# Optimization experiments

Measured on AMD Instinct MI355X. Metric: run time of the kernel, lower is better.

## Reference

```python
import jax, jax.numpy as jnp
import numpy as np

N, E = 50000, 800000
IN_D, HID, H1, OUT_D, H2, EDGE_D = 64, 16, 8, 64, 2, 1
NEG_SLOPE = 0.2


def gatv2_layer(x, src, dst, edge_attr, Wl, Wr, We, att, bias, concat):
    """PyG GATv2Conv (add_self_loops=False, share_weights=False), eval mode (no dropout)."""
    n = x.shape[0]
    H, C = att.shape
    xl = (x @ Wl).reshape(n, H, C)            # source transform
    xr = (x @ Wr).reshape(n, H, C)            # target transform
    ee = (edge_attr @ We).reshape(-1, H, C)   # edge embedding
    z = jax.nn.leaky_relu(xl[src] + xr[dst] + ee, NEG_SLOPE)  # [E,H,C]
    score = jnp.einsum('ehc,hc->eh', z, att)                  # [E,H]
    # softmax over incoming edges per target node
    m = jax.ops.segment_max(score, dst, num_segments=n)
    m = jnp.where(jnp.isfinite(m), m, 0.0)
    a = jnp.exp(score - m[dst])
    denom = jax.ops.segment_sum(a, dst, num_segments=n)
    alpha = a / (denom[dst] + 1e-16)                          # [E,H]
    msg = xl[src] * alpha[..., None]                          # [E,H,C]
    out = jax.ops.segment_sum(msg, dst, num_segments=n)       # [N,H,C]
    if concat:
        return out.reshape(n, H * C) + bias
    return out.mean(axis=1) + bias


def layer_norm(x, g, b):
    mu = x.mean(-1, keepdims=True)
    var = ((x - mu) ** 2).mean(-1, keepdims=True)
    return (x - mu) * jax.lax.rsqrt(var + 1e-5) * g + b


def setup_inputs() -> dict:
    key = jax.random.key(0)
    ks = jax.random.split(key, 24)
    def w(k, *shape):
        fan_in = shape[0]
        return jax.random.normal(k, shape, dtype=jnp.float32) * (1.0 / np.sqrt(fan_in))
    inp = {
        'x': jax.random.normal(ks[0], (N, IN_D), dtype=jnp.float32),
        'edge_index': jax.random.randint(ks[1], (2, E), 0, N, dtype=jnp.int64),
        'edge_attr': jax.random.normal(ks[2], (E, EDGE_D), dtype=jnp.float32),
        # layer 1 (heads=8, out=16, concat)
        'w1_l': w(ks[3], IN_D, H1 * HID), 'w1_r': w(ks[4], IN_D, H1 * HID),
        'w1_e': w(ks[5], EDGE_D, H1 * HID),
        'att1': jax.random.normal(ks[6], (H1, HID), dtype=jnp.float32) * 0.1,
        'b1': jnp.zeros((H1 * HID,), dtype=jnp.float32),
        # layer 2 (heads=2, out=64, mean)
        'w2_l': w(ks[7], H1 * HID, H2 * OUT_D), 'w2_r': w(ks[8], H1 * HID, H2 * OUT_D),
        'w2_e': w(ks[9], EDGE_D, H2 * OUT_D),
        'att2': jax.random.normal(ks[10], (H2, OUT_D), dtype=jnp.float32) * 0.1,
        'b2': jnp.zeros((OUT_D,), dtype=jnp.float32),
        # classifier: Linear + LayerNorm + GELU + ResidualBlockv2
        'wc': w(ks[11], OUT_D, OUT_D), 'bc': jnp.zeros((OUT_D,), dtype=jnp.float32),
        'ln_g': jnp.ones((OUT_D,), dtype=jnp.float32), 'ln_b': jnp.zeros((OUT_D,), dtype=jnp.float32),
        'wr': w(ks[12], OUT_D, OUT_D), 'br': jnp.zeros((OUT_D,), dtype=jnp.float32),
        'lnr_g': jnp.ones((OUT_D,), dtype=jnp.float32), 'lnr_b': jnp.zeros((OUT_D,), dtype=jnp.float32),
    }
    return inp


def reference(x, edge_index, edge_attr, w1_l, w1_r, w1_e, att1, b1,
              w2_l, w2_r, w2_e, att2, b2, wc, bc, ln_g, ln_b, wr, br, lnr_g, lnr_b):
    src, dst = edge_index[0], edge_index[1]
    h = jax.nn.relu(gatv2_layer(x, src, dst, edge_attr, w1_l, w1_r, w1_e, att1, b1, True))
    h = jax.nn.relu(gatv2_layer(h, src, dst, edge_attr, w2_l, w2_r, w2_e, att2, b2, False))
    h = jax.nn.gelu(layer_norm(h @ wc + bc, ln_g, ln_b), approximate=False)
    # ResidualBlockv2: Linear -> LayerNorm -> GELU with residual skip
    h = h + jax.nn.gelu(layer_norm(h @ wr + br, lnr_g, lnr_b), approximate=False)
    return h
```

## Files before the change

kernel.cpp:

```cpp
#include <hip/hip_runtime.h>
#include <math.h>

#define NNODE 50000
#define NEDGE 800000
#define NBLK_SCAN 196

__device__ __forceinline__ float wsum64(float v) {
    #pragma unroll
    for (int m = 32; m >= 1; m >>= 1) v += __shfl_xor(v, m, 64);
    return v;
}

__device__ __forceinline__ float gelu_exact(float x) {
    return 0.5f * x * (1.0f + erff(x * 0.70710678118654752f));
}

__device__ __forceinline__ float lrelu(float z) { return z > 0.f ? z : 0.2f * z; }

__global__ void fill_u32(unsigned* __restrict__ p, unsigned v, int n) {
    int i = blockIdx.x * blockDim.x + threadIdx.x;
    if (i < n) p[i] = v;
}

__global__ __launch_bounds__(256) void build_deg(const int* __restrict__ ei, int* __restrict__ deg) {
    int e = blockIdx.x * 256 + threadIdx.x;
    if (e >= NEDGE) return;
    atomicAdd(&deg[ei[NEDGE + e]], 1);
}

__global__ __launch_bounds__(256) void scan1(const int* __restrict__ deg,
                                             int* __restrict__ partial,
                                             int* __restrict__ bsum) {
    __shared__ int tmp[256];
    int t = threadIdx.x;
    int gid = blockIdx.x * 256 + t;
    int v = (gid < NNODE) ? deg[gid] : 0;
    tmp[t] = v;
    __syncthreads();
    #pragma unroll
    for (int off = 1; off < 256; off <<= 1) {
        int u = (t >= off) ? tmp[t - off] : 0;
        __syncthreads();
        tmp[t] += u;
        __syncthreads();
    }
    if (gid < NNODE) partial[gid] = tmp[t] - v;
    if (t == 255) bsum[blockIdx.x] = tmp[255];
}

__global__ __launch_bounds__(256) void scan2(int* __restrict__ bsum, int* __restrict__ boff) {
    __shared__ int tmp[256];
    int t = threadIdx.x;
    int v = (t < NBLK_SCAN) ? bsum[t] : 0;
    tmp[t] = v;
    __syncthreads();
    #pragma unroll
    for (int off = 1; off < 256; off <<= 1) {
        int u = (t >= off) ? tmp[t - off] : 0;
        __syncthreads();
        tmp[t] += u;
        __syncthreads();
    }
    if (t < NBLK_SCAN) boff[t] = tmp[t] - v;
}

__global__ __launch_bounds__(256) void scan3(const int* __restrict__ partial,
                                             const int* __restrict__ boff,
                                             int* __restrict__ base,
                                             int* __restrict__ cursor) {
    int gid = blockIdx.x * 256 + threadIdx.x;
    if (gid < NNODE) {
        int b = partial[gid] + boff[blockIdx.x];
        base[gid] = b;
        cursor[gid] = b;
    }
    if (gid == 0) base[NNODE] = NEDGE;
}

__global__ __launch_bounds__(256) void scatter_edges(const int* __restrict__ ei,
                                                     const float* __restrict__ ea,
                                                     int* __restrict__ cursor,
                                                     int2* __restrict__ se) {
    int e = blockIdx.x * 256 + threadIdx.x;
    if (e >= NEDGE) return;
    int d = ei[NEDGE + e];
    int i = atomicAdd(&cursor[d], 1);
    se[i] = make_int2(ei[e], __float_as_int(ea[e]));
}

template<int K>
__global__ __launch_bounds__(256) void node_xform(const float* __restrict__ in,
                                                  const float* __restrict__ wl,
                                                  const float* __restrict__ wr,
                                                  float* __restrict__ xl,
                                                  float* __restrict__ xr) {
    __shared__ float xrow[32][K];
    int t = threadIdx.x;
    int n0 = blockIdx.x * 32;
    for (int idx = t; idx < 32 * (K / 4); idx += 256) {
        int row = idx / (K / 4), c4 = idx % (K / 4);
        float4 v = make_float4(0.f, 0.f, 0.f, 0.f);
        if (n0 + row < NNODE) v = ((const float4*)(in + (size_t)(n0 + row) * K))[c4];
        ((float4*)xrow[row])[c4] = v;
    }
    __syncthreads();
    int cg = t & 63, ns = t >> 6;
    const float* wsel = (cg < 32) ? wl : wr;
    float* osel = (cg < 32) ? xl : xr;
    int ccol = (cg & 31) * 4;
    const float* wp = wsel + ccol;
    const float* xbase = xrow[ns * 8];
    float4 acc[8];
    #pragma unroll
    for (int k = 0; k < 8; ++k) acc[k] = make_float4(0.f, 0.f, 0.f, 0.f);
    for (int i = 0; i < K; i += 4) {
        float4 w0 = *(const float4*)(wp + (size_t)(i + 0) * 128);
        float4 w1 = *(const float4*)(wp + (size_t)(i + 1) * 128);
        float4 w2 = *(const float4*)(wp + (size_t)(i + 2) * 128);
        float4 w3 = *(const float4*)(wp + (size_t)(i + 3) * 128);
        #pragma unroll
        for (int k = 0; k < 8; ++k) {
            float4 xv = *(const float4*)(xbase + (size_t)k * K + i);
            acc[k].x += xv.x * w0.x + xv.y * w1.x + xv.z * w2.x + xv.w * w3.x;
            acc[k].y += xv.x * w0.y + xv.y * w1.y + xv.z * w2.y + xv.w * w3.y;
            acc[k].z += xv.x * w0.z + xv.y * w1.z + xv.z * w2.z + xv.w * w3.z;
            acc[k].w += xv.x * w0.w + xv.y * w1.w + xv.z * w2.w + xv.w * w3.w;
        }
    }
    #pragma unroll
    for (int k = 0; k < 8; ++k) {
        int n = n0 + ns * 8 + k;
        if (n < NNODE) *(float4*)(osel + (size_t)n * 128 + ccol) = acc[k];
    }
}

__global__ __launch_bounds__(256) void fused1(const int* __restrict__ base,
                                              const int2* __restrict__ se,
                                              const float* __restrict__ xl,
                                              const float* __restrict__ xr,
                                              const float* __restrict__ w1e,
                                              const float* __restrict__ att1,
                                              const float* __restrict__ b1,
                                              float* __restrict__ h1) {
    int t = threadIdx.x;
    int wv = t >> 6, ln = t & 63;
    int half = ln >> 5, sub = ln & 31;
    int n = blockIdx.x * 4 + wv;
    int ch = sub * 4;
    float4 xrv = *(const float4*)(xr + (size_t)n * 128 + ch);
    float4 wev = *(const float4*)(w1e + ch);
    float4 atv = *(const float4*)(att1 + ch);
    int i0 = base[n], i1 = base[n + 1];
    float m = -1e30f, den = 0.f;
    float4 o = make_float4(0.f, 0.f, 0.f, 0.f);
    int i = i0 + half;
    if (i < i1) {
        int2 r = se[i];
        float4 xv = *(const float4*)(xl + (size_t)r.x * 128 + ch);
        float a = __int_as_float(r.y);
        for (i += 2; i < i1; i += 2) {
            int2 rn = se[i];
            float4 nxv = *(const float4*)(xl + (size_t)rn.x * 128 + ch);
            float na = __int_as_float(rn.y);
            float part = lrelu(fmaf(a, wev.x, xv.x + xrv.x)) * atv.x
                       + lrelu(fmaf(a, wev.y, xv.y + xrv.y)) * atv.y
                       + lrelu(fmaf(a, wev.z, xv.z + xrv.z)) * atv.z
                       + lrelu(fmaf(a, wev.w, xv.w + xrv.w)) * atv.w;
            part += __shfl_xor(part, 1, 64);
            part += __shfl_xor(part, 2, 64);
            float mn = fmaxf(m, part);
            float sc = __expf(m - mn);
            float p  = __expf(part - mn);
            den = den * sc + p;
            o.x = o.x * sc + p * xv.x;
            o.y = o.y * sc + p * xv.y;
            o.z = o.z * sc + p * xv.z;
            o.w = o.w * sc + p * xv.w;
            m = mn;
            xv = nxv; a = na;
        }
        float part = lrelu(fmaf(a, wev.x, xv.x + xrv.x)) * atv.x
                   + lrelu(fmaf(a, wev.y, xv.y + xrv.y)) * atv.y
                   + lrelu(fmaf(a, wev.z, xv.z + xrv.z)) * atv.z
                   + lrelu(fmaf(a, wev.w, xv.w + xrv.w)) * atv.w;
        part += __shfl_xor(part, 1, 64);
        part += __shfl_xor(part, 2, 64);
        float mn = fmaxf(m, part);
        float sc = __expf(m - mn);
        float p  = __expf(part - mn);
        den = den * sc + p;
        o.x = o.x * sc + p * xv.x;
        o.y = o.y * sc + p * xv.y;
        o.z = o.z * sc + p * xv.z;
        o.w = o.w * sc + p * xv.w;
        m = mn;
    }
    float m2   = __shfl_xor(m, 32, 64);
    float den2 = __shfl_xor(den, 32, 64);
    float4 o2;
    o2.x = __shfl_xor(o.x, 32, 64);
    o2.y = __shfl_xor(o.y, 32, 64);
    o2.z = __shfl_xor(o.z, 32, 64);
    o2.w = __shfl_xor(o.w, 32, 64);
    float mn = fmaxf(m, m2);
    float s1 = __expf(m - mn), s2 = __expf(m2 - mn);
    den = den * s1 + den2 * s2;
    float inv = 1.f / (den + 1e-16f);
    if (half == 0) {
        float4 bv = *(const float4*)(b1 + ch);
        float4 res;
        res.x = fmaxf((o.x * s1 + o2.x * s2) * inv + bv.x, 0.f);
        res.y = fmaxf((o.y * s1 + o2.y * s2) * inv + bv.y, 0.f);
        res.z = fmaxf((o.z * s1 + o2.z * s2) * inv + bv.z, 0.f);
        res.w = fmaxf((o.w * s1 + o2.w * s2) * inv + bv.w, 0.f);
        *(float4*)(h1 + (size_t)n * 128 + ch) = res;
    }
}

__global__ __launch_bounds__(256) void fused2(const int* __restrict__ base,
                                              const int2* __restrict__ se,
                                              const float* __restrict__ xl,
                                              const float* __restrict__ xr,
                                              const float* __restrict__ w2e,
                                              const float* __restrict__ att2,
                                              const float* __restrict__ b2,
                                              float* __restrict__ h2) {
    int t = threadIdx.x;
    int wv = t >> 6, ln = t & 63;
    int half = ln >> 5, sub = ln & 31;
    int n = blockIdx.x * 4 + wv;
    int ch = sub * 4;
    float4 xrv = *(const float4*)(xr + (size_t)n * 128 + ch);
    float4 wev = *(const float4*)(w2e + ch);
    float4 atv = *(const float4*)(att2 + ch);
    int i0 = base[n], i1 = base[n + 1];
    float m = -1e30f, den = 0.f;
    float4 o = make_float4(0.f, 0.f, 0.f, 0.f);
    int i = i0 + half;
    if (i < i1) {
        int2 r = se[i];
        float4 xv = *(const float4*)(xl + (size_t)r.x * 128 + ch);
        float a = __int_as_float(r.y);
        for (i += 2; i < i1; i += 2) {
            int2 rn = se[i];
            float4 nxv = *(const float4*)(xl + (size_t)rn.x * 128 + ch);
            float na = __int_as_float(rn.y);
            float part = lrelu(fmaf(a, wev.x, xv.x + xrv.x)) * atv.x
                       + lrelu(fmaf(a, wev.y, xv.y + xrv.y)) * atv.y
                       + lrelu(fmaf(a, wev.z, xv.z + xrv.z)) * atv.z
                       + lrelu(fmaf(a, wev.w, xv.w + xrv.w)) * atv.w;
            part += __shfl_xor(part, 1, 64);
            part += __shfl_xor(part, 2, 64);
            part += __shfl_xor(part, 4, 64);
            part += __shfl_xor(part, 8, 64);
            float mn = fmaxf(m, part);
            float sc = __expf(m - mn);
            float p  = __expf(part - mn);
            den = den * sc + p;
            o.x = o.x * sc + p * xv.x;
            o.y = o.y * sc + p * xv.y;
            o.z = o.z * sc + p * xv.z;
            o.w = o.w * sc + p * xv.w;
            m = mn;
            xv = nxv; a = na;
        }
        float part = lrelu(fmaf(a, wev.x, xv.x + xrv.x)) * atv.x
                   + lrelu(fmaf(a, wev.y, xv.y + xrv.y)) * atv.y
                   + lrelu(fmaf(a, wev.z, xv.z + xrv.z)) * atv.z
                   + lrelu(fmaf(a, wev.w, xv.w + xrv.w)) * atv.w;
        part += __shfl_xor(part, 1, 64);
        part += __shfl_xor(part, 2, 64);
        part += __shfl_xor(part, 4, 64);
        part += __shfl_xor(part, 8, 64);
        float mn = fmaxf(m, part);
        float sc = __expf(m - mn);
        float p  = __expf(part - mn);
        den = den * sc + p;
        o.x = o.x * sc + p * xv.x;
        o.y = o.y * sc + p * xv.y;
        o.z = o.z * sc + p * xv.z;
        o.w = o.w * sc + p * xv.w;
        m = mn;
    }
    float m2   = __shfl_xor(m, 32, 64);
    float den2 = __shfl_xor(den, 32, 64);
    float4 o2;
    o2.x = __shfl_xor(o.x, 32, 64);
    o2.y = __shfl_xor(o.y, 32, 64);
    o2.z = __shfl_xor(o.z, 32, 64);
    o2.w = __shfl_xor(o.w, 32, 64);
    float mn = fmaxf(m, m2);
    float s1 = __expf(m - mn), s2 = __expf(m2 - mn);
    den = den * s1 + den2 * s2;
    float inv = 1.f / (den + 1e-16f);
    float4 v;
    v.x = (o.x * s1 + o2.x * s2) * inv;
    v.y = (o.y * s1 + o2.y * s2) * inv;
    v.z = (o.z * s1 + o2.z * s2) * inv;
    v.w = (o.w * s1 + o2.w * s2) * inv;
    float4 u;
    u.x = __shfl_xor(v.x, 16, 64);
    u.y = __shfl_xor(v.y, 16, 64);
    u.z = __shfl_xor(v.z, 16, 64);
    u.w = __shfl_xor(v.w, 16, 64);
    if (half == 0 && sub < 16) {
        float4 bv = *(const float4*)(b2 + ch);
        float4 res;
        res.x = fmaxf(0.5f * (v.x + u.x) + bv.x, 0.f);
        res.y = fmaxf(0.5f * (v.y + u.y) + bv.y, 0.f);
        res.z = fmaxf(0.5f * (v.z + u.z) + bv.z, 0.f);
        res.w = fmaxf(0.5f * (v.w + u.w) + bv.w, 0.f);
        *(float4*)(h2 + (size_t)n * 64 + ch) = res;
    }
}

__global__ __launch_bounds__(256) void classifier(const float* __restrict__ h2,
                                                  const float* __restrict__ wc,
                                                  const float* __restrict__ bc,
                                                  const float* __restrict__ lng,
                                                  const float* __restrict__ lnb,
                                                  const float* __restrict__ wr,
                                                  const float* __restrict__ br,
                                                  const float* __restrict__ lrg,
                                                  const float* __restrict__ lrb,
                                                  float* __restrict__ out) {
    __shared__ float rowA[4][64];
    __shared__ float rowB[4][64];
    int t = threadIdx.x;
    int wv = t >> 6, ln = t & 63;
    int n = blockIdx.x * 4 + wv;
    rowA[wv][ln] = h2[(size_t)n * 64 + ln];
    __syncthreads();
    float acc = bc[ln];
    #pragma unroll 8
    for (int i = 0; i < 64; ++i) acc += rowA[wv][i] * wc[i * 64 + ln];
    float mu = wsum64(acc) * (1.f / 64.f);
    float dv = acc - mu;
    float var = wsum64(dv * dv) * (1.f / 64.f);
    float y = dv * rsqrtf(var + 1e-5f) * lng[ln] + lnb[ln];
    float g1 = gelu_exact(y);
    rowB[wv][ln] = g1;
    __syncthreads();
    float acc2 = br[ln];
    #pragma unroll 8
    for (int i = 0; i < 64; ++i) acc2 += rowB[wv][i] * wr[i * 64 + ln];
    float mu2 = wsum64(acc2) * (1.f / 64.f);
    float dv2 = acc2 - mu2;
    float var2 = wsum64(dv2 * dv2) * (1.f / 64.f);
    float y2 = dv2 * rsqrtf(var2 + 1e-5f) * lrg[ln] + lrb[ln];
    float g2 = gelu_exact(y2);
    out[(size_t)n * 64 + ln] = g1 + g2;
}

extern "C" void kernel_launch(void* const* d_in, const int* in_sizes, int n_in,
                              void* d_out, int out_size, void* d_ws, size_t ws_size,
                              hipStream_t stream) {
    const float* x    = (const float*)d_in[0];
    const int*   ei   = (const int*)d_in[1];
    const float* ea   = (const float*)d_in[2];
    const float* w1l  = (const float*)d_in[3];
    const float* w1r  = (const float*)d_in[4];
    const float* w1e  = (const float*)d_in[5];
    const float* att1 = (const float*)d_in[6];
    const float* b1   = (const float*)d_in[7];
    const float* w2l  = (const float*)d_in[8];
    const float* w2r  = (const float*)d_in[9];
    const float* w2e  = (const float*)d_in[10];
    const float* att2 = (const float*)d_in[11];
    const float* b2   = (const float*)d_in[12];
    const float* wc   = (const float*)d_in[13];
    const float* bc   = (const float*)d_in[14];
    const float* lng  = (const float*)d_in[15];
    const float* lnb  = (const float*)d_in[16];
    const float* wr   = (const float*)d_in[17];
    const float* br   = (const float*)d_in[18];
    const float* lrg  = (const float*)d_in[19];
    const float* lrb  = (const float*)d_in[20];

    float* ws = (float*)d_ws;
    const size_t N128 = (size_t)NNODE * 128;
    float* xl = ws;
    float* xr = xl + N128;
    float* h1 = xr + N128;
    float* h2 = h1 + N128;
    int2*  se      = (int2*)(h2 + (size_t)NNODE * 64);
    int*   deg     = (int*)(se + NEDGE);
    int*   partial = deg + NNODE;
    int*   base    = partial + NNODE;
    int*   cursor  = base + NNODE + 1;
    int*   bsum    = cursor + NNODE;
    int*   boff    = bsum + 256;

    const int EB  = NEDGE / 256;
    const int NBX = (NNODE + 31) / 32;
    const int NB4 = NNODE / 4;

    fill_u32<<<NBLK_SCAN, 256, 0, stream>>>((unsigned*)deg, 0u, NNODE);
    build_deg<<<EB, 256, 0, stream>>>(ei, deg);
    scan1<<<NBLK_SCAN, 256, 0, stream>>>(deg, partial, bsum);
    scan2<<<1, 256, 0, stream>>>(bsum, boff);
    scan3<<<NBLK_SCAN, 256, 0, stream>>>(partial, boff, base, cursor);
    scatter_edges<<<EB, 256, 0, stream>>>(ei, ea, cursor, se);

    node_xform<64><<<NBX, 256, 0, stream>>>(x, w1l, w1r, xl, xr);
    fused1<<<NB4, 256, 0, stream>>>(base, se, xl, xr, w1e, att1, b1, h1);

    node_xform<128><<<NBX, 256, 0, stream>>>(h1, w2l, w2r, xl, xr);
    fused2<<<NB4, 256, 0, stream>>>(base, se, xl, xr, w2e, att2, b2, h2);

    classifier<<<NB4, 256, 0, stream>>>(h2, wc, bc, lng, lnb, wr, br, lrg, lrb,
                                        (float*)d_out);
}
```

Before: 351.6 us.

## Fuse layer-2 aggregation with classifier, widen edge parallelism, single-block scan

The layer-2 GATv2 aggregation kernel and the classifier are merged, so h2 stays in shared memory and its global write and reload go away. Both aggregation kernels now process four edges in parallel per wave with 8 channels per lane, and the online softmax skips the rescale when no lane's score exceeds the running max by more than a threshold. The three-kernel degree scan is replaced by a single-block serial-chunk scan. Risks are the single-block scan being slow, since each thread walks about 196 degrees serially, and higher register pressure from the wider per-lane state.

```diff
diff --git a/kernel.cpp b/kernel.cpp
--- a/kernel.cpp
+++ b/kernel.cpp
@@ -3,7 +3,7 @@
 
 #define NNODE 50000
 #define NEDGE 800000
-#define NBLK_SCAN 196
+#define NBLK 196
 
 __device__ __forceinline__ float wsum64(float v) {
     #pragma unroll
@@ -15,7 +15,63 @@
     return 0.5f * x * (1.0f + erff(x * 0.70710678118654752f));
 }
 
-__device__ __forceinline__ float lrelu(float z) { return z > 0.f ? z : 0.2f * z; }
+__device__ __forceinline__ float part8(float4 xa, float4 xb, float a,
+                                       float4 we0, float4 we1,
+                                       float4 at0, float4 at1,
+                                       float4 xr0, float4 xr1) {
+    float z0 = fmaf(a, we0.x, xa.x + xr0.x);
+    float z1 = fmaf(a, we0.y, xa.y + xr0.y);
+    float z2 = fmaf(a, we0.z, xa.z + xr0.z);
+    float z3 = fmaf(a, we0.w, xa.w + xr0.w);
+    float z4 = fmaf(a, we1.x, xb.x + xr1.x);
+    float z5 = fmaf(a, we1.y, xb.y + xr1.y);
+    float z6 = fmaf(a, we1.z, xb.z + xr1.z);
+    float z7 = fmaf(a, we1.w, xb.w + xr1.w);
+    float s01 = fmaxf(z0, 0.2f * z0) * at0.x + fmaxf(z1, 0.2f * z1) * at0.y;
+    float s23 = fmaxf(z2, 0.2f * z2) * at0.z + fmaxf(z3, 0.2f * z3) * at0.w;
+    float s45 = fmaxf(z4, 0.2f * z4) * at1.x + fmaxf(z5, 0.2f * z5) * at1.y;
+    float s67 = fmaxf(z6, 0.2f * z6) * at1.z + fmaxf(z7, 0.2f * z7) * at1.w;
+    return (s01 + s23) + (s45 + s67);
+}
+
+#define ONLINE_UPDATE(part, xa, xb)                                        \
+    if (__any((part) > m + 8.f)) {                                         \
+        float mn = fmaxf(m, (part));                                       \
+        float sc = __expf(m - mn);                                         \
+        float p  = __expf((part) - mn);                                    \
+        den = den * sc + p;                                                \
+        oa.x = oa.x * sc + p * (xa).x; oa.y = oa.y * sc + p * (xa).y;      \
+        oa.z = oa.z * sc + p * (xa).z; oa.w = oa.w * sc + p * (xa).w;      \
+        ob.x = ob.x * sc + p * (xb).x; ob.y = ob.y * sc + p * (xb).y;      \
+        ob.z = ob.z * sc + p * (xb).z; ob.w = ob.w * sc + p * (xb).w;      \
+        m = mn;                                                            \
+    } else {                                                               \
+        float p = __expf((part) - m);                                      \
+        den += p;                                                          \
+        oa.x = fmaf(p, (xa).x, oa.x); oa.y = fmaf(p, (xa).y, oa.y);        \
+        oa.z = fmaf(p, (xa).z, oa.z); oa.w = fmaf(p, (xa).w, oa.w);        \
+        ob.x = fmaf(p, (xb).x, ob.x); ob.y = fmaf(p, (xb).y, ob.y);        \
+        ob.z = fmaf(p, (xb).z, ob.z); ob.w = fmaf(p, (xb).w, ob.w);        \
+    }
+
+#define MERGE_STATE(D)                                                     \
+    {                                                                      \
+        float m2 = __shfl_xor(m, D, 64);                                   \
+        float d2 = __shfl_xor(den, D, 64);                                 \
+        float4 pa, pb;                                                     \
+        pa.x = __shfl_xor(oa.x, D, 64); pa.y = __shfl_xor(oa.y, D, 64);    \
+        pa.z = __shfl_xor(oa.z, D, 64); pa.w = __shfl_xor(oa.w, D, 64);    \
+        pb.x = __shfl_xor(ob.x, D, 64); pb.y = __shfl_xor(ob.y, D, 64);    \
+        pb.z = __shfl_xor(ob.z, D, 64); pb.w = __shfl_xor(ob.w, D, 64);    \
+        float mn = fmaxf(m, m2);                                           \
+        float s1 = __expf(m - mn), s2 = __expf(m2 - mn);                   \
+        den = den * s1 + d2 * s2;                                          \
+        oa.x = oa.x * s1 + pa.x * s2; oa.y = oa.y * s1 + pa.y * s2;        \
+        oa.z = oa.z * s1 + pa.z * s2; oa.w = oa.w * s1 + pa.w * s2;        \
+        ob.x = ob.x * s1 + pb.x * s2; ob.y = ob.y * s1 + pb.y * s2;        \
+        ob.z = ob.z * s1 + pb.z * s2; ob.w = ob.w * s1 + pb.w * s2;        \
+        m = mn;                                                            \
+    }
 
 __global__ void fill_u32(unsigned* __restrict__ p, unsigned v, int n) {
     int i = blockIdx.x * blockDim.x + threadIdx.x;
@@ -28,53 +84,32 @@
     atomicAdd(&deg[ei[NEDGE + e]], 1);
 }
 
-__global__ __launch_bounds__(256) void scan1(const int* __restrict__ deg,
-                                             int* __restrict__ partial,
-                                             int* __restrict__ bsum) {
-    __shared__ int tmp[256];
+__global__ __launch_bounds__(256) void scan_all(const int* __restrict__ deg,
+                                                int* __restrict__ base,
+                                                int* __restrict__ cursor) {
+    __shared__ int tsum[256];
     int t = threadIdx.x;
-    int gid = blockIdx.x * 256 + t;
-    int v = (gid < NNODE) ? deg[gid] : 0;
-    tmp[t] = v;
+    const int CH = (NNODE + 255) / 256;
+    int s0 = t * CH, s1 = min(s0 + CH, NNODE);
+    int s = 0;
+    for (int i = s0; i < s1; ++i) s += deg[i];
+    tsum[t] = s;
     __syncthreads();
     #pragma unroll
     for (int off = 1; off < 256; off <<= 1) {
-        int u = (t >= off) ? tmp[t - off] : 0;
+        int u = (t >= off) ? tsum[t - off] : 0;
         __syncthreads();
-        tmp[t] += u;
+        tsum[t] += u;
         __syncthreads();
     }
-    if (gid < NNODE) partial[gid] = tmp[t] - v;
-    if (t == 255) bsum[blockIdx.x] = tmp[255];
-}
-
-__global__ __launch_bounds__(256) void scan2(int* __restrict__ bsum, int* __restrict__ boff) {
-    __shared__ int tmp[256];
-    int t = threadIdx.x;
-    int v = (t < NBLK_SCAN) ? bsum[t] : 0;
-    tmp[t] = v;
-    __syncthreads();
-    #pragma unroll
-    for (int off = 1; off < 256; off <<= 1) {
-        int u = (t >= off) ? tmp[t - off] : 0;
-        __syncthreads();
-        tmp[t] += u;
-        __syncthreads();
-    }
-    if (t < NBLK_SCAN) boff[t] = tmp[t] - v;
-}
-
-__global__ __launch_bounds__(256) void scan3(const int* __restrict__ partial,
-                                             const int* __restrict__ boff,
-                                             int* __restrict__ base,
-                                             int* __restrict__ cursor) {
-    int gid = blockIdx.x * 256 + threadIdx.x;
-    if (gid < NNODE) {
-        int b = partial[gid] + boff[blockIdx.x];
-        base[gid] = b;
-        cursor[gid] = b;
-    }
-    if (gid == 0) base[NNODE] = NEDGE;
+    int run = tsum[t] - s;
+    for (int i = s0; i < s1; ++i) {
+        int d = deg[i];
+        base[i] = run;
+        cursor[i] = run;
+        run += d;
+    }
+    if (t == 0) base[NNODE] = NEDGE;
 }
 
 __global__ __launch_bounds__(256) void scatter_edges(const int* __restrict__ ei,
@@ -144,196 +179,147 @@
                                               float* __restrict__ h1) {
     int t = threadIdx.x;
     int wv = t >> 6, ln = t & 63;
-    int half = ln >> 5, sub = ln & 31;
+    int q = ln >> 4, sub = ln & 15;
     int n = blockIdx.x * 4 + wv;
-    int ch = sub * 4;
-    float4 xrv = *(const float4*)(xr + (size_t)n * 128 + ch);
-    float4 wev = *(const float4*)(w1e + ch);
-    float4 atv = *(const float4*)(att1 + ch);
+    int ch = sub * 8;
+    float4 xr0 = *(const float4*)(xr + (size_t)n * 128 + ch);
+    float4 xr1 = *(const float4*)(xr + (size_t)n * 128 + ch + 4);
+    float4 we0 = *(const float4*)(w1e + ch);
+    float4 we1 = *(const float4*)(w1e + ch + 4);
+    float4 at0 = *(const float4*)(att1 + ch);
+    float4 at1 = *(const float4*)(att1 + ch + 4);
     int i0 = base[n], i1 = base[n + 1];
     float m = -1e30f, den = 0.f;
-    float4 o = make_float4(0.f, 0.f, 0.f, 0.f);
-    int i = i0 + half;
+    float4 oa = make_float4(0.f, 0.f, 0.f, 0.f);
+    float4 ob = make_float4(0.f, 0.f, 0.f, 0.f);
+    int i = i0 + q;
     if (i < i1) {
         int2 r = se[i];
-        float4 xv = *(const float4*)(xl + (size_t)r.x * 128 + ch);
+        const float* xp = xl + (size_t)r.x * 128 + ch;
+        float4 xa = *(const float4*)xp, xb = *(const float4*)(xp + 4);
         float a = __int_as_float(r.y);
-        for (i += 2; i < i1; i += 2) {
+        for (i += 4; i < i1; i += 4) {
             int2 rn = se[i];
-            float4 nxv = *(const float4*)(xl + (size_t)rn.x * 128 + ch);
+            const float* xpn = xl + (size_t)rn.x * 128 + ch;
+            float4 nxa = *(const float4*)xpn, nxb = *(const float4*)(xpn + 4);
             float na = __int_as_float(rn.y);
-            float part = lrelu(fmaf(a, wev.x, xv.x + xrv.x)) * atv.x
-                       + lrelu(fmaf(a, wev.y, xv.y + xrv.y)) * atv.y
-                       + lrelu(fmaf(a, wev.z, xv.z + xrv.z)) * atv.z
-                       + lrelu(fmaf(a, wev.w, xv.w + xrv.w)) * atv.w;
+            float part = part8(xa, xb, a, we0, we1, at0, at1, xr0, xr1);
             part += __shfl_xor(part, 1, 64);
-            part += __shfl_xor(part, 2, 64);
-            float mn = fmaxf(m, part);
-            float sc = __expf(m - mn);
-            float p  = __expf(part - mn);
-            den = den * sc + p;
-            o.x = o.x * sc + p * xv.x;
-            o.y = o.y * sc + p * xv.y;
-            o.z = o.z * sc + p * xv.z;
-            o.w = o.w * sc + p * xv.w;
-            m = mn;
-            xv = nxv; a = na;
+            ONLINE_UPDATE(part, xa, xb);
+            xa = nxa; xb = nxb; a = na;
         }
-        float part = lrelu(fmaf(a, wev.x, xv.x + xrv.x)) * atv.x
-                   + lrelu(fmaf(a, wev.y, xv.y + xrv.y)) * atv.y
-                   + lrelu(fmaf(a, wev.z, xv.z + xrv.z)) * atv.z
-                   + lrelu(fmaf(a, wev.w, xv.w + xrv.w)) * atv.w;
+        float part = part8(xa, xb, a, we0, we1, at0, at1, xr0, xr1);
         part += __shfl_xor(part, 1, 64);
-        part += __shfl_xor(part, 2, 64);
-        float mn = fmaxf(m, part);
-        float sc = __expf(m - mn);
-        float p  = __expf(part - mn);
-        den = den * sc + p;
-        o.x = o.x * sc + p * xv.x;
-        o.y = o.y * sc + p * xv.y;
-        o.z = o.z * sc + p * xv.z;
-        o.w = o.w * sc + p * xv.w;
-        m = mn;
-    }
-    float m2   = __shfl_xor(m, 32, 64);
-    float den2 = __shfl_xor(den, 32, 64);
-    float4 o2;
-    o2.x = __shfl_xor(o.x, 32, 64);
-    o2.y = __shfl_xor(o.y, 32, 64);
-    o2.z = __shfl_xor(o.z, 32, 64);
-    o2.w = __shfl_xor(o.w, 32, 64);
-    float mn = fmaxf(m, m2);
-    float s1 = __expf(m - mn), s2 = __expf(m2 - mn);
-    den = den * s1 + den2 * s2;
-    float inv = 1.f / (den + 1e-16f);
-    if (half == 0) {
-        float4 bv = *(const float4*)(b1 + ch);
-        float4 res;
-        res.x = fmaxf((o.x * s1 + o2.x * s2) * inv + bv.x, 0.f);
-        res.y = fmaxf((o.y * s1 + o2.y * s2) * inv + bv.y, 0.f);
-        res.z = fmaxf((o.z * s1 + o2.z * s2) * inv + bv.z, 0.f);
-        res.w = fmaxf((o.w * s1 + o2.w * s2) * inv + bv.w, 0.f);
-        *(float4*)(h1 + (size_t)n * 128 + ch) = res;
-    }
-}
-
-__global__ __launch_bounds__(256) void fused2(const int* __restrict__ base,
-                                              const int2* __restrict__ se,
-                                              const float* __restrict__ xl,
-                                              const float* __restrict__ xr,
-                                              const float* __restrict__ w2e,
-                                              const float* __restrict__ att2,
-                                              const float* __restrict__ b2,
-                                              float* __restrict__ h2) {
+        ONLINE_UPDATE(part, xa, xb);
+    }
+    MERGE_STATE(16);
+    MERGE_STATE(32);
+    if (q == 0) {
+        float inv = 1.f / (den + 1e-16f);
+        float4 bv0 = *(const float4*)(b1 + ch);
+        float4 bv1 = *(const float4*)(b1 + ch + 4);
+        float4 ra, rb;
+        ra.x = fmaxf(oa.x * inv + bv0.x, 0.f);
+        ra.y = fmaxf(oa.y * inv + bv0.y, 0.f);
+        ra.z = fmaxf(oa.z * inv + bv0.z, 0.f);
+        ra.w = fmaxf(oa.w * inv + bv0.w, 0.f);
+        rb.x = fmaxf(ob.x * inv + bv1.x, 0.f);
+        rb.y = fmaxf(ob.y * inv + bv1.y, 0.f);
+        rb.z = fmaxf(ob.z * inv + bv1.z, 0.f);
+        rb.w = fmaxf(ob.w * inv + bv1.w, 0.f);
+        *(float4*)(h1 + (size_t)n * 128 + ch) = ra;
+        *(float4*)(h1 + (size_t)n * 128 + ch + 4) = rb;
+    }
+}
+
+__global__ __launch_bounds__(256) void fused2cls(const int* __restrict__ base,
+                                                 const int2* __restrict__ se,
+                                                 const float* __restrict__ xl,
+                                                 const float* __restrict__ xr,
+                                                 const float* __restrict__ w2e,
+                                                 const float* __restrict__ att2,
+                                                 const float* __restrict__ b2,
+                                                 const float* __restrict__ wc,
+                                                 const float* __restrict__ bc,
+                                                 const float* __restrict__ lng,
+                                                 const float* __restrict__ lnb,
+                                                 const float* __restrict__ wrr,
+                                                 const float* __restrict__ brr,
+                                                 const float* __restrict__ lrg,
+                                                 const float* __restrict__ lrb,
+                                                 float* __restrict__ out) {
+    __shared__ float rowH[4][64];
+    __shared__ float rowB[4][64];
     int t = threadIdx.x;
     int wv = t >> 6, ln = t & 63;
-    int half = ln >> 5, sub = ln & 31;
+    int q = ln >> 4, sub = ln & 15;
     int n = blockIdx.x * 4 + wv;
-    int ch = sub * 4;
-    float4 xrv = *(const float4*)(xr + (size_t)n * 128 + ch);
-    float4 wev = *(const float4*)(w2e + ch);
-    float4 atv = *(const float4*)(att2 + ch);
+    int ch = sub * 8;
+    float4 xr0 = *(const float4*)(xr + (size_t)n * 128 + ch);
+    float4 xr1 = *(const float4*)(xr + (size_t)n * 128 + ch + 4);
+    float4 we0 = *(const float4*)(w2e + ch);
+    float4 we1 = *(const float4*)(w2e + ch + 4);
+    float4 at0 = *(const float4*)(att2 + ch);
+    float4 at1 = *(const float4*)(att2 + ch + 4);
     int i0 = base[n], i1 = base[n + 1];
     float m = -1e30f, den = 0.f;
-    float4 o = make_float4(0.f, 0.f, 0.f, 0.f);
-    int i = i0 + half;
+    float4 oa = make_float4(0.f, 0.f, 0.f, 0.f);
+    float4 ob = make_float4(0.f, 0.f, 0.f, 0.f);
+    int i = i0 + q;
     if (i < i1) {
         int2 r = se[i];
-        float4 xv = *(const float4*)(xl + (size_t)r.x * 128 + ch);
+        const float* xp = xl + (size_t)r.x * 128 + ch;
+        float4 xa = *(const float4*)xp, xb = *(const float4*)(xp + 4);
         float a = __int_as_float(r.y);
-        for (i += 2; i < i1; i += 2) {
+        for (i += 4; i < i1; i += 4) {
             int2 rn = se[i];
-            float4 nxv = *(const float4*)(xl + (size_t)rn.x * 128 + ch);
+            const float* xpn = xl + (size_t)rn.x * 128 + ch;
+            float4 nxa = *(const float4*)xpn, nxb = *(const float4*)(xpn + 4);
             float na = __int_as_float(rn.y);
-            float part = lrelu(fmaf(a, wev.x, xv.x + xrv.x)) * atv.x
-                       + lrelu(fmaf(a, wev.y, xv.y + xrv.y)) * atv.y
-                       + lrelu(fmaf(a, wev.z, xv.z + xrv.z)) * atv.z
-                       + lrelu(fmaf(a, wev.w, xv.w + xrv.w)) * atv.w;
+            float part = part8(xa, xb, a, we0, we1, at0, at1, xr0, xr1);
             part += __shfl_xor(part, 1, 64);
             part += __shfl_xor(part, 2, 64);
             part += __shfl_xor(part, 4, 64);
-            part += __shfl_xor(part, 8, 64);
-            float mn = fmaxf(m, part);
-            float sc = __expf(m - mn);
-            float p  = __expf(part - mn);
-            den = den * sc + p;
-            o.x = o.x * sc + p * xv.x;
-            o.y = o.y * sc + p * xv.y;
-            o.z = o.z * sc + p * xv.z;
-            o.w = o.w * sc + p * xv.w;
-            m = mn;
-            xv = nxv; a = na;
+            ONLINE_UPDATE(part, xa, xb);
+            xa = nxa; xb = nxb; a = na;
         }
-        float part = lrelu(fmaf(a, wev.x, xv.x + xrv.x)) * atv.x
-                   + lrelu(fmaf(a, wev.y, xv.y + xrv.y)) * atv.y
-                   + lrelu(fmaf(a, wev.z, xv.z + xrv.z)) * atv.z
-                   + lrelu(fmaf(a, wev.w, xv.w + xrv.w)) * atv.w;
+        float part = part8(xa, xb, a, we0, we1, at0, at1, xr0, xr1);
         part += __shfl_xor(part, 1, 64);
         part += __shfl_xor(part, 2, 64);
         part += __shfl_xor(part, 4, 64);
-        part += __shfl_xor(part, 8, 64);
-        float mn = fmaxf(m, part);
-        float sc = __expf(m - mn);
-        float p  = __expf(part - mn);
-        den = den * sc + p;
-        o.x = o.x * sc + p * xv.x;
-        o.y = o.y * sc + p * xv.y;
-        o.z = o.z * sc + p * xv.z;
-        o.w = o.w * sc + p * xv.w;
-        m = mn;
-    }
-    float m2   = __shfl_xor(m, 32, 64);
-    float den2 = __shfl_xor(den, 32, 64);
-    float4 o2;
-    o2.x = __shfl_xor(o.x, 32, 64);
-    o2.y = __shfl_xor(o.y, 32, 64);
-    o2.z = __shfl_xor(o.z, 32, 64);
-    o2.w = __shfl_xor(o.w, 32, 64);
-    float mn = fmaxf(m, m2);
-    float s1 = __expf(m - mn), s2 = __expf(m2 - mn);
-    den = den * s1 + den2 * s2;
+        ONLINE_UPDATE(part, xa, xb);
+    }
+    MERGE_STATE(16);
+    MERGE_STATE(32);
     float inv = 1.f / (den + 1e-16f);
-    float4 v;
-    v.x = (o.x * s1 + o2.x * s2) * inv;
-    v.y = (o.y * s1 + o2.y * s2) * inv;
-    v.z = (o.z * s1 + o2.z * s2) * inv;
-    v.w = (o.w * s1 + o2.w * s2) * inv;
-    float4 u;
-    u.x = __shfl_xor(v.x, 16, 64);
-    u.y = __shfl_xor(v.y, 16, 64);
-    u.z = __shfl_xor(v.z, 16, 64);
-    u.w = __shfl_xor(v.w, 16, 64);
-    if (half == 0 && sub < 16) {
-        float4 bv = *(const float4*)(b2 + ch);
-        float4 res;
-        res.x = fmaxf(0.5f * (v.x + u.x) + bv.x, 0.f);
-        res.y = fmaxf(0.5f * (v.y + u.y) + bv.y, 0.f);
-        res.z = fmaxf(0.5f * (v.z + u.z) + bv.z, 0.f);
-        res.w = fmaxf(0.5f * (v.w + u.w) + bv.w, 0.f);
-        *(float4*)(h2 + (size_t)n * 64 + ch) = res;
-    }
-}
-
-__global__ __launch_bounds__(256) void classifier(const float* __restrict__ h2,
-                                                  const float* __restrict__ wc,
-                                                  const float* __restrict__ bc,
-                                                  const float* __restrict__ lng,
-                                                  const float* __restrict__ lnb,
-                                                  const float* __restrict__ wr,
-                                                  const float* __restrict__ br,
-                                                  const float* __restrict__ lrg,
-                                                  const float* __restrict__ lrb,
-                                                  float* __restrict__ out) {
-    __shared__ float rowA[4][64];
-    __shared__ float rowB[4][64];
-    int t = threadIdx.x;
-    int wv = t >> 6, ln = t & 63;
-    int n = blockIdx.x * 4 + wv;
-    rowA[wv][ln] = h2[(size_t)n * 64 + ln];
+    float4 va, vb;
+    va.x = oa.x * inv; va.y = oa.y * inv; va.z = oa.z * inv; va.w = oa.w * inv;
+    vb.x = ob.x * inv; vb.y = ob.y * inv; vb.z = ob.z * inv; vb.w = ob.w * inv;
+    float4 ua, ub;
+    ua.x = __shfl_xor(va.x, 8, 64); ua.y = __shfl_xor(va.y, 8, 64);
+    ua.z = __shfl_xor(va.z, 8, 64); ua.w = __shfl_xor(va.w, 8, 64);
+    ub.x = __shfl_xor(vb.x, 8, 64); ub.y = __shfl_xor(vb.y, 8, 64);
+    ub.z = __shfl_xor(vb.z, 8, 64); ub.w = __shfl_xor(vb.w, 8, 64);
+    if (q == 0 && sub < 8) {
+        int c = sub * 8;
+        float4 bv0 = *(const float4*)(b2 + c);
+        float4 bv1 = *(const float4*)(b2 + c + 4);
+        float4 ra, rb;
+        ra.x = fmaxf(0.5f * (va.x + ua.x) + bv0.x, 0.f);
+        ra.y = fmaxf(0.5f * (va.y + ua.y) + bv0.y, 0.f);
+        ra.z = fmaxf(0.5f * (va.z + ua.z) + bv0.z, 0.f);
+        ra.w = fmaxf(0.5f * (va.w + ua.w) + bv0.w, 0.f);
+        rb.x = fmaxf(0.5f * (vb.x + ub.x) + bv1.x, 0.f);
+        rb.y = fmaxf(0.5f * (vb.y + ub.y) + bv1.y, 0.f);
+        rb.z = fmaxf(0.5f * (vb.z + ub.z) + bv1.z, 0.f);
+        rb.w = fmaxf(0.5f * (vb.w + ub.w) + bv1.w, 0.f);
+        *(float4*)(&rowH[wv][c]) = ra;
+        *(float4*)(&rowH[wv][c + 4]) = rb;
+    }
     __syncthreads();
     float acc = bc[ln];
     #pragma unroll 8
-    for (int i = 0; i < 64; ++i) acc += rowA[wv][i] * wc[i * 64 + ln];
+    for (int j = 0; j < 64; ++j) acc += rowH[wv][j] * wc[j * 64 + ln];
     float mu = wsum64(acc) * (1.f / 64.f);
     float dv = acc - mu;
     float var = wsum64(dv * dv) * (1.f / 64.f);
@@ -341,9 +327,9 @@
     float g1 = gelu_exact(y);
     rowB[wv][ln] = g1;
     __syncthreads();
-    float acc2 = br[ln];
+    float acc2 = brr[ln];
     #pragma unroll 8
-    for (int i = 0; i < 64; ++i) acc2 += rowB[wv][i] * wr[i * 64 + ln];
+    for (int j = 0; j < 64; ++j) acc2 += rowB[wv][j] * wrr[j * 64 + ln];
     float mu2 = wsum64(acc2) * (1.f / 64.f);
     float dv2 = acc2 - mu2;
     float var2 = wsum64(dv2 * dv2) * (1.f / 64.f);
@@ -382,32 +368,25 @@
     float* xl = ws;
     float* xr = xl + N128;
     float* h1 = xr + N128;
-    float* h2 = h1 + N128;
-    int2*  se      = (int2*)(h2 + (size_t)NNODE * 64);
+    int2*  se      = (int2*)(h1 + N128);
     int*   deg     = (int*)(se + NEDGE);
-    int*   partial = deg + NNODE;
-    int*   base    = partial + NNODE;
+    int*   base    = deg + NNODE;
     int*   cursor  = base + NNODE + 1;
-    int*   bsum    = cursor + NNODE;
-    int*   boff    = bsum + 256;
 
     const int EB  = NEDGE / 256;
     const int NBX = (NNODE + 31) / 32;
     const int NB4 = NNODE / 4;
 
-    fill_u32<<<NBLK_SCAN, 256, 0, stream>>>((unsigned*)deg, 0u, NNODE);
+    fill_u32<<<NBLK, 256, 0, stream>>>((unsigned*)deg, 0u, NNODE);
     build_deg<<<EB, 256, 0, stream>>>(ei, deg);
-    scan1<<<NBLK_SCAN, 256, 0, stream>>>(deg, partial, bsum);
-    scan2<<<1, 256, 0, stream>>>(bsum, boff);
-    scan3<<<NBLK_SCAN, 256, 0, stream>>>(partial, boff, base, cursor);
+    scan_all<<<1, 256, 0, stream>>>(deg, base, cursor);
     scatter_edges<<<EB, 256, 0, stream>>>(ei, ea, cursor, se);
 
     node_xform<64><<<NBX, 256, 0, stream>>>(x, w1l, w1r, xl, xr);
     fused1<<<NB4, 256, 0, stream>>>(base, se, xl, xr, w1e, att1, b1, h1);
 
     node_xform<128><<<NBX, 256, 0, stream>>>(h1, w2l, w2r, xl, xr);
-    fused2<<<NB4, 256, 0, stream>>>(base, se, xl, xr, w2e, att2, b2, h2);
-
-    classifier<<<NB4, 256, 0, stream>>>(h2, wc, bc, lng, lnb, wr, br, lrg, lrb,
-                                        (float*)d_out);
-}
+    fused2cls<<<NB4, 256, 0, stream>>>(base, se, xl, xr, w2e, att2, b2,
+                                       wc, bc, lng, lnb, wr, br, lrg, lrb,
+                                       (float*)d_out);
+}
```

New measurement: 469.6 us. +33.6%, slower.
